# Optimization experiments

Measured on AMD Instinct MI355X. Metric: run time of the kernel, lower is better.

The kernel has to match this reference:

```python
import jax, jax.numpy as jnp
import numpy as np

N = 524288          # batch size
NUM_SD = 64         # socio-demographic chars
H = 128             # hidden size of TasteParams MLP
NUM_ALT_FEAT = 9    # alternative features
NUM_CLASSES = 3
# utility_structure: class k -> (start, end) column slice of x
SEGMENTS = [(0, 3), (3, 6), (6, 9)]


def setup_inputs() -> dict:
    key = jax.random.key(0)
    ks = jax.random.split(key, 8)
    s = 0.05
    return {
        "x": jax.random.normal(ks[0], (N, NUM_ALT_FEAT), jnp.float32),
        "z": jax.random.normal(ks[1], (N, NUM_SD), jnp.float32),
        "W1": jax.random.normal(ks[2], (NUM_SD, H), jnp.float32) * s,
        "b1": jax.random.normal(ks[3], (H,), jnp.float32) * s,
        "W2": jax.random.normal(ks[4], (H, H), jnp.float32) * s,
        "b2": jax.random.normal(ks[5], (H,), jnp.float32) * s,
        "W3": jax.random.normal(ks[6], (H, NUM_ALT_FEAT + NUM_CLASSES), jnp.float32) * s,
        "b3": jax.random.normal(ks[7], (NUM_ALT_FEAT + NUM_CLASSES,), jnp.float32) * s,
    }


def _forward(x, z, W1, b1, W2, b2, W3, b3):
    # TasteParams MLP: Linear-ReLU-Linear-ReLU-Linear
    h = jax.nn.relu(z @ W1 + b1)
    h = jax.nn.relu(h @ W2 + b2)
    b = h @ W3 + b3                        # (N, 12)
    # monotonic_constraints (num_classes==3, func_intercept=True)
    b = jnp.concatenate([
        -jax.nn.relu(-b[:, :6]),
        b[:, 6:7],
        -jax.nn.relu(-b[:, 7:9]),
        b[:, -NUM_CLASSES:],
    ], axis=1)
    taste = b[:, :NUM_ALT_FEAT]            # (N, 9)
    intercept = b[:, -NUM_CLASSES:]        # (N, 3)
    # MNL_layer with b: per-segment elementwise mult + reduce into logits column
    prod = x * taste                       # (N, 9)
    logits = jnp.stack(
        [prod[:, lo:hi].sum(axis=1) for (lo, hi) in SEGMENTS], axis=1
    )                                      # (N, 3)
    return logits + intercept


def reference(x, z, W1, b1, W2, b2, W3, b3):
    return _forward(x, z, W1, b1, W2, b2, W3, b3)
```

## Files before the change

### kernel.cpp

```cpp
#include <hip/hip_runtime.h>
#include <hip/hip_bf16.h>


typedef __bf16 bf16x8 __attribute__((ext_vector_type(8)));
typedef float  f32x16 __attribute__((ext_vector_type(16)));
typedef unsigned int uint2v __attribute__((ext_vector_type(2)));
typedef unsigned int uint4v __attribute__((ext_vector_type(4)));

#define MFMA32(a, b, c) __builtin_amdgcn_mfma_f32_32x32x16_bf16((a), (b), (c), 0, 0, 0)
#define PIN_AGPR(v) asm("" : "+a"(v))

#define SW3 0
#define SW1 1536
#define SW2 9728
#define SB1 26112
#define SB2 26240
#define SB3 26368
#define SMEM_ELTS 26384

#define NBLK    512
#define NTILE   16384
#define WSTRIDE (NBLK * 4)

__device__ __forceinline__ unsigned pkbf(float lo, float hi) {
  unsigned short lb = __builtin_bit_cast(unsigned short, (__bf16)lo);
  unsigned short hb = __builtin_bit_cast(unsigned short, (__bf16)hi);
  return ((unsigned)hb << 16) | (unsigned)lb;
}

template <int SUB>
__device__ __forceinline__ bf16x8 mk_bfrag(const f32x16 h) {
  constexpr int B = SUB * 8;
  unsigned p01 = pkbf(h[B + 0], h[B + 1]);
  unsigned p23 = pkbf(h[B + 2], h[B + 3]);
  unsigned p45 = pkbf(h[B + 4], h[B + 5]);
  unsigned p67 = pkbf(h[B + 6], h[B + 7]);
  unsigned d0, d1, d2, d3;
#if __has_builtin(__builtin_amdgcn_permlane32_swap)
  uint2v r1 = __builtin_amdgcn_permlane32_swap(p01, p45, false, false);
  uint2v r2 = __builtin_amdgcn_permlane32_swap(p23, p67, false, false);
  d0 = r1[0]; d2 = r1[1];
  d1 = r2[0]; d3 = r2[1];
#else
  int hi = (threadIdx.x >> 5) & 1;
  unsigned sp01 = (unsigned)__shfl_xor((int)p01, 32, 64);
  unsigned sp23 = (unsigned)__shfl_xor((int)p23, 32, 64);
  unsigned sp45 = (unsigned)__shfl_xor((int)p45, 32, 64);
  unsigned sp67 = (unsigned)__shfl_xor((int)p67, 32, 64);
  d0 = hi ? sp45 : p01;
  d2 = hi ? p45  : sp01;
  d1 = hi ? sp67 : p23;
  d3 = hi ? p67  : sp23;
#endif
  uint4v t; t[0] = d0; t[1] = d1; t[2] = d2; t[3] = d3;
  return __builtin_bit_cast(bf16x8, t);
}

__device__ __forceinline__ bf16x8 ldw(const __bf16* sm, int vaddr, int imm) {
  return *(const bf16x8*)((const char*)sm + vaddr + imm);
}

__device__ __forceinline__ bf16x8 biasA(__bf16 v) {
  bf16x8 f;
  #pragma unroll
  for (int i = 0; i < 8; ++i) f[i] = (__bf16)0.0f;
  f[0] = v;
  return f;
}

__global__ __launch_bounds__(256, 2)
void tastenet_kernel(const float* __restrict__ x, const float* __restrict__ z,
                     const float* __restrict__ W1, const float* __restrict__ b1,
                     const float* __restrict__ W2, const float* __restrict__ b2,
                     const float* __restrict__ W3, const float* __restrict__ b3,
                     float* __restrict__ out) {
  __shared__ __align__(16) __bf16 sm[SMEM_ELTS];
  const int tid = threadIdx.x;
  unsigned* smw = (unsigned*)sm;

  for (int i = tid; i < 4096; i += 256) {
    int m = i & 127, k = (i >> 7) * 2;
    smw[SW1 / 2 + m * 32 + (((k >> 3) ^ (m & 7)) << 2) + ((k >> 1) & 3)] =
        pkbf(W1[k * 128 + m], W1[(k + 1) * 128 + m]);
  }
  for (int i = tid; i < 8192; i += 256) {
    int m = i & 127, k = (i >> 7) * 2;
    smw[SW2 / 2 + m * 64 + (((k >> 3) ^ (m & 7)) << 2) + ((k >> 1) & 3)] =
        pkbf(W2[k * 128 + m], W2[(k + 1) * 128 + m]);
  }
  for (int i = tid; i < 768; i += 256) {
    int kk = i / 12, m = i - kk * 12, k = kk * 2;
    smw[SW3 / 2 + m * 64 + (((k >> 3) ^ (m & 7)) << 2) + ((k >> 1) & 3)] =
        pkbf(W3[k * 12 + m], W3[(k + 1) * 12 + m]);
  }
  if (tid < 128) { sm[SB1 + tid] = (__bf16)b1[tid]; sm[SB2 + tid] = (__bf16)b2[tid]; }
  if (tid < 12)  sm[SB3 + tid] = (__bf16)b3[tid];
  __syncthreads();

  const int wave = tid >> 6;
  const int lane = tid & 63;
  const int q    = lane >> 5;
  const int n    = lane & 31;
  const int s8   = n & 7;
  const int eq   = q ^ (s8 & 1);
  const int sh   = s8 >> 1;

  int aw1[4], aw2[4];
  #pragma unroll
  for (int j = 0; j < 4; ++j) {
    aw1[j] = n * 128 + eq * 16 + 32 * (j ^ sh);
    aw2[j] = n * 256 + eq * 16 + 32 * (j ^ sh);
  }

  __bf16 bv1[4], bv2[4], bv3;
  #pragma unroll
  for (int f = 0; f < 4; ++f) {
    bv1[f] = (q == 0) ? sm[SB1 + f * 32 + n] : (__bf16)0.0f;
    bv2[f] = (q == 0) ? sm[SB2 + f * 32 + n] : (__bf16)0.0f;
  }
  bv3 = (q == 0 && n < 12) ? sm[SB3 + n] : (__bf16)0.0f;

  bf16x8 ones;
  #pragma unroll
  for (int i = 0; i < 8; ++i) ones[i] = (__bf16)0.0f;
  if (q == 0) ones[0] = (__bf16)1.0f;

  const int wid = blockIdx.x * 4 + wave;

  float4 zv[8];
  {
    const float* zr = z + ((long)wid * 32 + n) * 64;
    #pragma unroll
    for (int kt = 0; kt < 4; ++kt) {
      zv[2 * kt]     = *(const float4*)(zr + kt * 16 + q * 8);
      zv[2 * kt + 1] = *(const float4*)(zr + kt * 16 + q * 8 + 4);
    }
  }

  #pragma unroll 1
  for (int t = wid; t < NTILE; t += WSTRIDE) {
    const long row = (long)t * 32 + n;

    const float* xr = x + row * 9;
    float xv0 = xr[q * 4 + 0], xv1 = xr[q * 4 + 1];
    float xv2 = xr[q * 4 + 2], xv3 = xr[q * 4 + 3];
    float xv4 = xr[8];

    bf16x8 bz[4];
    #pragma unroll
    for (int kt = 0; kt < 4; ++kt) {
      float4 a = zv[2 * kt], b = zv[2 * kt + 1];
      bf16x8 f;
      f[0] = (__bf16)a.x; f[1] = (__bf16)a.y; f[2] = (__bf16)a.z; f[3] = (__bf16)a.w;
      f[4] = (__bf16)b.x; f[5] = (__bf16)b.y; f[6] = (__bf16)b.z; f[7] = (__bf16)b.w;
      bz[kt] = f;
    }

    if (t + WSTRIDE < NTILE) {
      const float* zr = z + ((long)(t + WSTRIDE) * 32 + n) * 64;
      #pragma unroll
      for (int kt = 0; kt < 4; ++kt) {
        zv[2 * kt]     = *(const float4*)(zr + kt * 16 + q * 8);
        zv[2 * kt + 1] = *(const float4*)(zr + kt * 16 + q * 8 + 4);
      }
    }

    bf16x8 bf2[8];
    #pragma unroll
    for (int fp = 0; fp < 2; ++fp) {
      f32x16 aA, aB;
      #pragma unroll
      for (int i = 0; i < 16; ++i) { aA[i] = 0.0f; aB[i] = 0.0f; }
      PIN_AGPR(aA); PIN_AGPR(aB);
      #pragma unroll
      for (int kt = 0; kt < 4; ++kt) {
        aA = MFMA32(ldw(sm, aw1[kt], SW1 * 2 + (2 * fp + 0) * 4096), bz[kt], aA);
        aB = MFMA32(ldw(sm, aw1[kt], SW1 * 2 + (2 * fp + 1) * 4096), bz[kt], aB);
      }
      aA = MFMA32(biasA(bv1[2 * fp + 0]), ones, aA);
      aB = MFMA32(biasA(bv1[2 * fp + 1]), ones, aB);
      #pragma unroll
      for (int i = 0; i < 16; ++i) { aA[i] = fmaxf(aA[i], 0.0f); aB[i] = fmaxf(aB[i], 0.0f); }
      bf2[4 * fp + 0] = mk_bfrag<0>(aA);
      bf2[4 * fp + 1] = mk_bfrag<1>(aA);
      bf2[4 * fp + 2] = mk_bfrag<0>(aB);
      bf2[4 * fp + 3] = mk_bfrag<1>(aB);
    }

    f32x16 acc3;
    #pragma unroll
    for (int i = 0; i < 16; ++i) acc3[i] = 0.0f;
    PIN_AGPR(acc3);
    #pragma unroll
    for (int fp = 0; fp < 2; ++fp) {
      f32x16 aA, aB;
      #pragma unroll
      for (int i = 0; i < 16; ++i) { aA[i] = 0.0f; aB[i] = 0.0f; }
      PIN_AGPR(aA); PIN_AGPR(aB);
      #pragma unroll
      for (int kt = 0; kt < 8; ++kt) {
        aA = MFMA32(ldw(sm, aw2[kt & 3], SW2 * 2 + (2 * fp + 0) * 8192 + 128 * (kt >> 2)),
                    bf2[kt], aA);
        aB = MFMA32(ldw(sm, aw2[kt & 3], SW2 * 2 + (2 * fp + 1) * 8192 + 128 * (kt >> 2)),
                    bf2[kt], aB);
      }
      aA = MFMA32(biasA(bv2[2 * fp + 0]), ones, aA);
      aB = MFMA32(biasA(bv2[2 * fp + 1]), ones, aB);
      #pragma unroll
      for (int i = 0; i < 16; ++i) { aA[i] = fmaxf(aA[i], 0.0f); aB[i] = fmaxf(aB[i], 0.0f); }
      acc3 = MFMA32(ldw(sm, aw2[0], SW3 * 2 + 128 * fp), mk_bfrag<0>(aA), acc3);
      acc3 = MFMA32(ldw(sm, aw2[1], SW3 * 2 + 128 * fp), mk_bfrag<1>(aA), acc3);
      acc3 = MFMA32(ldw(sm, aw2[2], SW3 * 2 + 128 * fp), mk_bfrag<0>(aB), acc3);
      acc3 = MFMA32(ldw(sm, aw2[3], SW3 * 2 + 128 * fp), mk_bfrag<1>(aB), acc3);
    }
    acc3 = MFMA32(biasA(bv3), ones, acc3);

    float t0 = acc3[0], t1 = acc3[1], t2 = acc3[2], t3 = acc3[3];
    float t4 = acc3[4], t5 = acc3[5], t6 = acc3[6], t7 = acc3[7];
    float o0 = 0.f, o1 = 0.f, o2 = 0.f, g1v = 0.f, g2v = 0.f;
    if (q == 0) {
      t0 = fminf(t0, 0.0f); t1 = fminf(t1, 0.0f);
      t2 = fminf(t2, 0.0f); t3 = fminf(t3, 0.0f);
      t4 = fminf(t4, 0.0f);
      o0 = xv0 * t0 + xv1 * t1 + xv2 * t2 + t5;
      o1 = xv3 * t3 + t6;
      o2 = xv4 * t4 + t7;
    } else {
      t0 = fminf(t0, 0.0f); t1 = fminf(t1, 0.0f);
      t3 = fminf(t3, 0.0f);
      g1v = xv0 * t0 + xv1 * t1;
      g2v = xv2 * t2 + xv3 * t3;
    }
    float a1v = __shfl_xor(g1v, 32, 64);
    float a2v = __shfl_xor(g2v, 32, 64);
    if (q == 0) {
      float* op = out + row * 3;
      op[0] = o0;
      op[1] = o1 + a1v;
      op[2] = o2 + a2v;
    }
  }
}

extern "C" void kernel_launch(void* const* d_in, const int* in_sizes, int n_in,
                              void* d_out, int out_size, void* d_ws, size_t ws_size,
                              hipStream_t stream) {
  const float* x  = (const float*)d_in[0];
  const float* z  = (const float*)d_in[1];
  const float* W1 = (const float*)d_in[2];
  const float* b1 = (const float*)d_in[3];
  const float* W2 = (const float*)d_in[4];
  const float* b2 = (const float*)d_in[5];
  const float* W3 = (const float*)d_in[6];
  const float* b3 = (const float*)d_in[7];
  tastenet_kernel<<<dim3(NBLK), dim3(256), 0, stream>>>(
      x, z, W1, b1, W2, b2, W3, b3, (float*)d_out);
}
```

Before: 235.4 us.

## Drop register prefetch of z, load x late, and raise block count

Removes the software-pipelined register prefetch of the next z tile and loads the current tile's z at the top of each iteration instead. The x loads move to the epilogue, after the MLP. Grid size goes from 512 to 768 blocks. The aim is to free registers so more waves stay resident and rely on occupancy, not explicit prefetch, to hide memory latency. The risk is exposed global load latency per tile if occupancy does not actually rise.

Measured after the change: 261.2 us. 11.0% more time.

```diff
diff --git a/kernel.cpp b/kernel.cpp
--- a/kernel.cpp
+++ b/kernel.cpp
@@ -18,7 +18,7 @@
 #define SB3 26368
 #define SMEM_ELTS 26384
 
-#define NBLK    512
+#define NBLK    768
 #define NTILE   16384
 #define WSTRIDE (NBLK * 4)
 
@@ -127,42 +127,25 @@
 
   const int wid = blockIdx.x * 4 + wave;
 
-  float4 zv[8];
-  {
-    const float* zr = z + ((long)wid * 32 + n) * 64;
-    #pragma unroll
-    for (int kt = 0; kt < 4; ++kt) {
-      zv[2 * kt]     = *(const float4*)(zr + kt * 16 + q * 8);
-      zv[2 * kt + 1] = *(const float4*)(zr + kt * 16 + q * 8 + 4);
-    }
-  }
-
   #pragma unroll 1
   for (int t = wid; t < NTILE; t += WSTRIDE) {
     const long row = (long)t * 32 + n;
 
-    const float* xr = x + row * 9;
-    float xv0 = xr[q * 4 + 0], xv1 = xr[q * 4 + 1];
-    float xv2 = xr[q * 4 + 2], xv3 = xr[q * 4 + 3];
-    float xv4 = xr[8];
-
+    const float* zr = z + row * 64;
+    float4 zt[8];
+    #pragma unroll
+    for (int kt = 0; kt < 4; ++kt) {
+      zt[2 * kt]     = *(const float4*)(zr + kt * 16 + q * 8);
+      zt[2 * kt + 1] = *(const float4*)(zr + kt * 16 + q * 8 + 4);
+    }
     bf16x8 bz[4];
     #pragma unroll
     for (int kt = 0; kt < 4; ++kt) {
-      float4 a = zv[2 * kt], b = zv[2 * kt + 1];
+      float4 a = zt[2 * kt], b = zt[2 * kt + 1];
       bf16x8 f;
       f[0] = (__bf16)a.x; f[1] = (__bf16)a.y; f[2] = (__bf16)a.z; f[3] = (__bf16)a.w;
       f[4] = (__bf16)b.x; f[5] = (__bf16)b.y; f[6] = (__bf16)b.z; f[7] = (__bf16)b.w;
       bz[kt] = f;
-    }
-
-    if (t + WSTRIDE < NTILE) {
-      const float* zr = z + ((long)(t + WSTRIDE) * 32 + n) * 64;
-      #pragma unroll
-      for (int kt = 0; kt < 4; ++kt) {
-        zv[2 * kt]     = *(const float4*)(zr + kt * 16 + q * 8);
-        zv[2 * kt + 1] = *(const float4*)(zr + kt * 16 + q * 8 + 4);
-      }
     }
 
     bf16x8 bf2[8];
@@ -215,6 +198,7 @@
     }
     acc3 = MFMA32(biasA(bv3), ones, acc3);
 
+    const float* xr = x + row * 9;
     float t0 = acc3[0], t1 = acc3[1], t2 = acc3[2], t3 = acc3[3];
     float t4 = acc3[4], t5 = acc3[5], t6 = acc3[6], t7 = acc3[7];
     float o0 = 0.f, o1 = 0.f, o2 = 0.f, g1v = 0.f, g2v = 0.f;
@@ -222,14 +206,14 @@
       t0 = fminf(t0, 0.0f); t1 = fminf(t1, 0.0f);
       t2 = fminf(t2, 0.0f); t3 = fminf(t3, 0.0f);
       t4 = fminf(t4, 0.0f);
-      o0 = xv0 * t0 + xv1 * t1 + xv2 * t2 + t5;
-      o1 = xv3 * t3 + t6;
-      o2 = xv4 * t4 + t7;
+      o0 = xr[0] * t0 + xr[1] * t1 + xr[2] * t2 + t5;
+      o1 = xr[3] * t3 + t6;
+      o2 = xr[8] * t4 + t7;
     } else {
       t0 = fminf(t0, 0.0f); t1 = fminf(t1, 0.0f);
       t3 = fminf(t3, 0.0f);
-      g1v = xv0 * t0 + xv1 * t1;
-      g2v = xv2 * t2 + xv3 * t3;
+      g1v = xr[4] * t0 + xr[5] * t1;
+      g2v = xr[6] * t2 + xr[7] * t3;
     }
     float a1v = __shfl_xor(g1v, 32, 64);
     float a2v = __shfl_xor(g2v, 32, 64);
```
